# Kernel optimization log

Measured on AMD Instinct MI355X. Metric: run time of the kernel, lower is better.

Reference implementation:

```python
import jax, jax.numpy as jnp
import numpy as np

GAMMA = 0.99
EPS = 1e-8
N = 16777216  # flattened reward count


def setup_inputs() -> dict:
    key = jax.random.key(0)
    rewards = jax.random.normal(key, (N,), dtype=jnp.float32)
    return {"rewards": rewards}


def reference(rewards):
    # Sequential recurrence: R_t = gamma*R_{t-1} + r_t, Welford stats over R_t,
    # scaled[i] = r_i / max(std_t, eps), std_t = sqrt(var_sum/count) (1.0 if count < 2).
    flat = rewards.reshape(-1)

    def step(carry, r):
        R, cnt, mean, var_sum = carry
        R = GAMMA * R + r
        cnt = cnt + 1.0
        delta = R - mean
        mean = mean + delta / cnt
        var_sum = var_sum + delta * (R - mean)
        std = jnp.where(cnt < 2.0, jnp.float32(1.0), jnp.sqrt(var_sum / cnt))
        std = jnp.maximum(std, jnp.float32(EPS))
        return (R, cnt, mean, var_sum), r / std

    init = (jnp.float32(0.0), jnp.float32(0.0), jnp.float32(0.0), jnp.float32(0.0))
    _, scaled = jax.lax.scan(step, init, flat)
    return scaled.reshape(rewards.shape)
```

## Files before the change

### kernel.cpp

```cpp
#include <hip/hip_runtime.h>
#include <math.h>

#define THREADS 256
#define GAMMA 0.99

typedef float vf4 __attribute__((ext_vector_type(4)));

template<int LPT>
__device__ __forceinline__ int padi(int i) { return i + (i >> LPT); }

template<int NW>
__device__ __forceinline__ void block_compose_excl(int tid, double g, double v,
                                                   double& eg, double& ev,
                                                   double* lg, double* lv) {
    const int lane = tid & 63, wave = tid >> 6;
    double ig = g, iv = v;
#pragma unroll
    for (int k = 1; k < 64; k <<= 1) {
        double og = __shfl_up(ig, k);
        double ov = __shfl_up(iv, k);
        if (lane >= k) { iv = fma(ig, ov, iv); ig *= og; }
    }
    double weg = __shfl_up(ig, 1);
    double wev = __shfl_up(iv, 1);
    if (lane == 0) { weg = 1.0; wev = 0.0; }
    if (lane == 63) { lg[wave] = ig; lv[wave] = iv; }
    __syncthreads();
    double bg = 1.0, bv = 0.0;
    for (int w = 0; w < wave; ++w) { bv = fma(lg[w], bv, lv[w]); bg *= lg[w]; }
    eg = weg * bg;
    ev = fma(weg, bv, wev);
}

template<int NW>
__device__ __forceinline__ void block_add_excl2(int tid, double a, double b,
                                                double& ea, double& eb,
                                                double* la, double* lb) {
    const int lane = tid & 63, wave = tid >> 6;
    double ia = a, ib = b;
#pragma unroll
    for (int k = 1; k < 64; k <<= 1) {
        double oa = __shfl_up(ia, k);
        double ob = __shfl_up(ib, k);
        if (lane >= k) { ia += oa; ib += ob; }
    }
    double wea = __shfl_up(ia, 1);
    double web = __shfl_up(ib, 1);
    if (lane == 0) { wea = 0.0; web = 0.0; }
    if (lane == 63) { la[wave] = ia; lb[wave] = ib; }
    __syncthreads();
    double ba = 0.0, bb = 0.0;
    for (int w = 0; w < wave; ++w) { ba += la[w]; bb += lb[w]; }
    ea = wea + ba;
    eb = web + bb;
}

template<int PT, int LPT>
__global__ __launch_bounds__(THREADS) void rs_phase1(const float* __restrict__ in,
                                                     double* __restrict__ agg, int nchunk) {
    constexpr int CHUNKE = THREADS * PT;
    __shared__ double lg[4], lv[4], r1[4], r2[4], r3[4];
    const int tid = threadIdx.x, lane = tid & 63, wave = tid >> 6;
    const int chunk = blockIdx.x;
    const float* src = in + (size_t)chunk * CHUNKE + (size_t)tid * PT;

    float rv[PT];
#pragma unroll
    for (int q = 0; q < PT / 4; ++q) {
        const float4 t = ((const float4*)src)[q];
        rv[4 * q] = t.x; rv[4 * q + 1] = t.y; rv[4 * q + 2] = t.z; rv[4 * q + 3] = t.w;
    }
    const float gf = (float)GAMMA;
    float p = 0.f, psum = 0.f, pq = 0.f, p2 = 0.f, gp = 1.f;
#pragma unroll
    for (int j = 0; j < PT; ++j) {
        p = fmaf(gf, p, rv[j]);
        gp *= gf;
        psum += p;
        pq = fmaf(gp, p, pq);
        p2 = fmaf(p, p, p2);
    }
    const double g = GAMMA;
    double gPT = g;
#pragma unroll
    for (int e = 0; e < LPT; ++e) gPT *= gPT;

    double eg, ev;
    block_compose_excl<4>(tid, gPT, (double)p, eg, ev, lg, lv);
    const double rho = ev, gexc = eg;

    const double G1 = g * (1.0 - gPT) / (1.0 - g);
    const double G2 = g * g * (1.0 - gPT * gPT) / (1.0 - g * g);
    double c1 = fma(rho, G1, (double)psum);
    double c2 = gexc * fma(rho, G2, (double)pq);
    double c3 = fma(rho * rho, G2, fma(2.0 * rho, (double)pq, (double)p2));
#pragma unroll
    for (int k = 32; k > 0; k >>= 1) {
        c1 += __shfl_down(c1, k);
        c2 += __shfl_down(c2, k);
        c3 += __shfl_down(c3, k);
    }
    if (lane == 0) { r1[wave] = c1; r2[wave] = c2; r3[wave] = c3; }
    __syncthreads();
    if (tid == 0) {
        double A = 0.0;
#pragma unroll
        for (int w = 0; w < 4; ++w) A = fma(lg[w], A, lv[w]);
        agg[4 * (size_t)chunk + 0] = A;
        agg[4 * (size_t)chunk + 1] = r1[0] + r1[1] + r1[2] + r1[3];
        agg[4 * (size_t)chunk + 2] = r2[0] + r2[1] + r2[2] + r2[3];
        agg[4 * (size_t)chunk + 3] = r3[0] + r3[1] + r3[2] + r3[3];
    }
}

template<int CPT, int LOG2CHUNK>
__global__ __launch_bounds__(1024) void rs_phase2(const double* __restrict__ agg,
                                                  double* __restrict__ car, int nchunk) {
    __shared__ double lg[16], lv[16], la[16], lb[16];
    const int t = threadIdx.x;
    const double g = GAMMA;
    double gC = g;
#pragma unroll
    for (int e = 0; e < LOG2CHUNK; ++e) gC *= gC;

    double A[CPT], Ps[CPT], Pq[CPT], P2[CPT];
    const int c0 = t * CPT;
#pragma unroll
    for (int i = 0; i < CPT; ++i) {
        const int c = c0 + i;
        const bool ok = c < nchunk;
        A[i]  = ok ? agg[4 * (size_t)c + 0] : 0.0;
        Ps[i] = ok ? agg[4 * (size_t)c + 1] : 0.0;
        Pq[i] = ok ? agg[4 * (size_t)c + 2] : 0.0;
        P2[i] = ok ? agg[4 * (size_t)c + 3] : 0.0;
    }
    double mg = 1.0, mv = 0.0;
#pragma unroll
    for (int i = 0; i < CPT; ++i) { mv = fma(gC, mv, A[i]); mg *= gC; }

    double eg, ev;
    block_compose_excl<16>(t, mg, mv, eg, ev, lg, lv);

    const double G1C = g * (1.0 - gC) / (1.0 - g);
    const double G2C = g * g * (1.0 - gC * gC) / (1.0 - g * g);
    double Rin[CPT + 1];
    Rin[0] = ev;
    double s1[CPT], s2[CPT];
#pragma unroll
    for (int i = 0; i < CPT; ++i) {
        s1[i] = fma(Rin[i], G1C, Ps[i]);
        s2[i] = fma(Rin[i] * Rin[i], G2C, fma(2.0 * Rin[i], Pq[i], P2[i]));
        Rin[i + 1] = fma(gC, Rin[i], A[i]);
    }
    double ts1 = 0.0, ts2 = 0.0;
#pragma unroll
    for (int i = 0; i < CPT; ++i) { ts1 += s1[i]; ts2 += s2[i]; }
    double ea, eb;
    block_add_excl2<16>(t, ts1, ts2, ea, eb, la, lb);
#pragma unroll
    for (int i = 0; i < CPT; ++i) {
        const int c = c0 + i;
        if (c < nchunk) {
            car[3 * (size_t)c + 0] = Rin[i];
            car[3 * (size_t)c + 1] = ea;
            car[3 * (size_t)c + 2] = eb;
        }
        ea += s1[i];
        eb += s2[i];
    }
}

template<int PT, int LPT>
__global__ __launch_bounds__(THREADS) void rs_phase3(const float* __restrict__ in,
                                                     float* __restrict__ out,
                                                     const double* __restrict__ car, int nchunk) {
    constexpr int CHUNKE = THREADS * PT;
    __shared__ float sbuf[CHUNKE + THREADS];
    __shared__ double lg[4], lv[4], la[4], lb[4];
    const int tid = threadIdx.x;
    const int chunk = blockIdx.x;
    const float* src = in + (size_t)chunk * CHUNKE + (size_t)tid * PT;

    float rv[PT];
#pragma unroll
    for (int q = 0; q < PT / 4; ++q) {
        const float4 t = ((const float4*)src)[q];
        rv[4 * q] = t.x; rv[4 * q + 1] = t.y; rv[4 * q + 2] = t.z; rv[4 * q + 3] = t.w;
    }
    const float gf = (float)GAMMA;
    float p = 0.f, psum = 0.f, pq = 0.f, p2 = 0.f, gp = 1.f;
#pragma unroll
    for (int j = 0; j < PT; ++j) {
        p = fmaf(gf, p, rv[j]);
        gp *= gf;
        psum += p;
        pq = fmaf(gp, p, pq);
        p2 = fmaf(p, p, p2);
    }
    const double g = GAMMA;
    double gPT = g;
#pragma unroll
    for (int e = 0; e < LPT; ++e) gPT *= gPT;

    double eg, ev;
    block_compose_excl<4>(tid, gPT, (double)p, eg, ev, lg, lv);

    const double RinC = car[3 * (size_t)chunk + 0];
    const double S1C  = car[3 * (size_t)chunk + 1];
    const double S2C  = car[3 * (size_t)chunk + 2];
    const double rin  = fma(eg, RinC, ev);

    const double G1 = g * (1.0 - gPT) / (1.0 - g);
    const double G2 = g * g * (1.0 - gPT * gPT) / (1.0 - g * g);
    const double s1 = fma(rin, G1, (double)psum);
    const double s2 = fma(rin * rin, G2, fma(2.0 * rin, (double)pq, (double)p2));
    double ea, eb;
    block_add_excl2<4>(tid, s1, s2, ea, eb, la, lb);
    const double S1b = S1C + ea;
    const double S2b = S2C + eb;

    const int a0 = padi<LPT>(tid * PT);

    if (chunk == 0) {
        double R = rin, S1 = S1b, S2 = S2b;
        const size_t gbase = (size_t)tid * PT;
        for (int j = 0; j < PT; ++j) {
            const float rf = rv[j];
            R = fma(g, R, (double)rf);
            S1 += R;
            S2 = fma(R, R, S2);
            float ov;
            if (gbase + j == 0) {
                ov = rf;
            } else {
                const double cnt = (double)(gbase + j + 1);
                const double inv = 1.0 / cnt;
                const double mean = S1 * inv;
                double var = fma(S2, inv, -(mean * mean));
                var = var > 0.0 ? var : 0.0;
                double sd = sqrt(var);
                sd = sd > 1e-8 ? sd : 1e-8;
                ov = (float)((double)rf / sd);
            }
            sbuf[a0 + j] = ov;
        }
    } else {
        float R = (float)rin;
        float ls1 = 0.f, ls2 = 0.f;
        const float S1bf = (float)S1b, S2bf = (float)S2b;
        const float base_cnt = (float)((size_t)chunk * CHUNKE + (size_t)tid * PT);
#pragma unroll
        for (int j = 0; j < PT; ++j) {
            const float rf = rv[j];
            R = fmaf(gf, R, rf);
            ls1 += R;
            ls2 = fmaf(R, R, ls2);
            const float cnt = base_cnt + (float)(j + 1);
            const float S1f = S1bf + ls1;
            const float S2f = S2bf + ls2;
            float t = fmaf(S2f, cnt, -(S1f * S1f));
            t = fmaxf(t, 1e-12f);
            sbuf[a0 + j] = rf * cnt * __builtin_amdgcn_rsqf(t);
        }
    }
    __syncthreads();

    float* dst = out + (size_t)chunk * CHUNKE;
    for (int i = tid * 4; i < CHUNKE; i += THREADS * 4) {
        const int pp = padi<LPT>(i);
        vf4 v;
        v.x = sbuf[pp]; v.y = sbuf[pp + 1]; v.z = sbuf[pp + 2]; v.w = sbuf[pp + 3];
        __builtin_nontemporal_store(v, (vf4*)(dst + i));
    }
}

extern "C" void kernel_launch(void* const* d_in, const int* in_sizes, int n_in,
                              void* d_out, int out_size, void* d_ws, size_t ws_size,
                              hipStream_t stream) {
    (void)n_in; (void)out_size;
    const float* in = (const float*)d_in[0];
    float* out = (float*)d_out;
    double* ws = (double*)d_ws;
    const int n = in_sizes[0];

    const int nc = n / 4096;
    if ((n % 4096) == 0 && nc >= 1 && nc <= 4096 &&
        ws_size >= (size_t)7 * nc * sizeof(double)) {
        double* agg = ws;
        double* car = ws + 4 * (size_t)nc;
        rs_phase1<16, 4><<<nc, THREADS, 0, stream>>>(in, agg, nc);
        rs_phase2<4, 12><<<1, 1024, 0, stream>>>(agg, car, nc);
        rs_phase3<16, 4><<<nc, THREADS, 0, stream>>>(in, out, car, nc);
    } else {
        const int nc64 = n / 16384;
        double* agg = ws;
        double* car = ws + 4 * (size_t)nc64;
        rs_phase1<64, 6><<<nc64, THREADS, 0, stream>>>(in, agg, nc64);
        rs_phase2<4, 14><<<1, 1024, 0, stream>>>(agg, car, nc64);
        rs_phase3<64, 6><<<nc64, THREADS, 0, stream>>>(in, out, car, nc64);
    }
}
```

Measured before the change: 55.02 us.

## Fuse chunk-carry scan into phase-1 kernel via last-block atomic counter

Merges the separate single-block carry-scan kernel into the tail of the per-chunk aggregation kernel. Each block increments a global counter after writing its aggregates, and the last block to finish performs the cross-chunk scan and writes the carries. This removes one kernel launch and its dependency gap. In exchange it adds a memset launch and does the scan with 256 threads instead of 1024, so each thread has a longer serial loop and reads the aggregates from global memory twice.

```diff
diff --git a/kernel.cpp b/kernel.cpp
--- a/kernel.cpp
+++ b/kernel.cpp
@@ -55,11 +55,14 @@
     eb = web + bb;
 }
 
-template<int PT, int LPT>
-__global__ __launch_bounds__(THREADS) void rs_phase1(const float* __restrict__ in,
-                                                     double* __restrict__ agg, int nchunk) {
+template<int PT, int LPT, int LOG2CH>
+__global__ __launch_bounds__(THREADS) void rs_phase12(const float* __restrict__ in,
+                                                      double* __restrict__ agg,
+                                                      double* __restrict__ car,
+                                                      int* __restrict__ counter, int nchunk) {
     constexpr int CHUNKE = THREADS * PT;
-    __shared__ double lg[4], lv[4], r1[4], r2[4], r3[4];
+    __shared__ double lg[4], lv[4], r1[4], r2[4], r3[4], la[4], lb[4];
+    __shared__ int is_last;
     const int tid = threadIdx.x, lane = tid & 63, wave = tid >> 6;
     const int chunk = blockIdx.x;
     const float* src = in + (size_t)chunk * CHUNKE + (size_t)tid * PT;
@@ -110,63 +113,54 @@
         agg[4 * (size_t)chunk + 1] = r1[0] + r1[1] + r1[2] + r1[3];
         agg[4 * (size_t)chunk + 2] = r2[0] + r2[1] + r2[2] + r2[3];
         agg[4 * (size_t)chunk + 3] = r3[0] + r3[1] + r3[2] + r3[3];
-    }
-}
-
-template<int CPT, int LOG2CHUNK>
-__global__ __launch_bounds__(1024) void rs_phase2(const double* __restrict__ agg,
-                                                  double* __restrict__ car, int nchunk) {
-    __shared__ double lg[16], lv[16], la[16], lb[16];
-    const int t = threadIdx.x;
-    const double g = GAMMA;
+        __threadfence();
+        const int prev = atomicAdd(counter, 1);
+        is_last = (prev == nchunk - 1) ? 1 : 0;
+    }
+    __syncthreads();
+    if (!is_last) return;
+
+    __threadfence();
     double gC = g;
 #pragma unroll
-    for (int e = 0; e < LOG2CHUNK; ++e) gC *= gC;
-
-    double A[CPT], Ps[CPT], Pq[CPT], P2[CPT];
-    const int c0 = t * CPT;
-#pragma unroll
-    for (int i = 0; i < CPT; ++i) {
-        const int c = c0 + i;
-        const bool ok = c < nchunk;
-        A[i]  = ok ? agg[4 * (size_t)c + 0] : 0.0;
-        Ps[i] = ok ? agg[4 * (size_t)c + 1] : 0.0;
-        Pq[i] = ok ? agg[4 * (size_t)c + 2] : 0.0;
-        P2[i] = ok ? agg[4 * (size_t)c + 3] : 0.0;
-    }
-    double mg = 1.0, mv = 0.0;
-#pragma unroll
-    for (int i = 0; i < CPT; ++i) { mv = fma(gC, mv, A[i]); mg *= gC; }
-
-    double eg, ev;
-    block_compose_excl<16>(t, mg, mv, eg, ev, lg, lv);
-
+    for (int e = 0; e < LOG2CH; ++e) gC *= gC;
     const double G1C = g * (1.0 - gC) / (1.0 - g);
     const double G2C = g * g * (1.0 - gC * gC) / (1.0 - g * g);
-    double Rin[CPT + 1];
-    Rin[0] = ev;
-    double s1[CPT], s2[CPT];
-#pragma unroll
-    for (int i = 0; i < CPT; ++i) {
-        s1[i] = fma(Rin[i], G1C, Ps[i]);
-        s2[i] = fma(Rin[i] * Rin[i], G2C, fma(2.0 * Rin[i], Pq[i], P2[i]));
-        Rin[i + 1] = fma(gC, Rin[i], A[i]);
-    }
-    double ts1 = 0.0, ts2 = 0.0;
-#pragma unroll
-    for (int i = 0; i < CPT; ++i) { ts1 += s1[i]; ts2 += s2[i]; }
+
+    const int CPT2 = (nchunk + THREADS - 1) / THREADS;
+    const int b_lo = tid * CPT2;
+    const int b_hi = min(nchunk, b_lo + CPT2);
+
+    double mg = 1.0, mv = 0.0;
+    for (int c = b_lo; c < b_hi; ++c) { mv = fma(gC, mv, agg[4 * (size_t)c]); mg *= gC; }
+    double eg2, ev2;
+    block_compose_excl<4>(tid, mg, mv, eg2, ev2, lg, lv);
+
+    double Rin = ev2, ts1 = 0.0, ts2 = 0.0;
+    for (int c = b_lo; c < b_hi; ++c) {
+        const double Ac = agg[4 * (size_t)c + 0];
+        const double Ps = agg[4 * (size_t)c + 1];
+        const double Pq = agg[4 * (size_t)c + 2];
+        const double P2 = agg[4 * (size_t)c + 3];
+        ts1 += fma(Rin, G1C, Ps);
+        ts2 += fma(Rin * Rin, G2C, fma(2.0 * Rin, Pq, P2));
+        Rin = fma(gC, Rin, Ac);
+    }
     double ea, eb;
-    block_add_excl2<16>(t, ts1, ts2, ea, eb, la, lb);
-#pragma unroll
-    for (int i = 0; i < CPT; ++i) {
-        const int c = c0 + i;
-        if (c < nchunk) {
-            car[3 * (size_t)c + 0] = Rin[i];
-            car[3 * (size_t)c + 1] = ea;
-            car[3 * (size_t)c + 2] = eb;
-        }
-        ea += s1[i];
-        eb += s2[i];
+    block_add_excl2<4>(tid, ts1, ts2, ea, eb, la, lb);
+
+    Rin = ev2;
+    for (int c = b_lo; c < b_hi; ++c) {
+        const double Ac = agg[4 * (size_t)c + 0];
+        const double Ps = agg[4 * (size_t)c + 1];
+        const double Pq = agg[4 * (size_t)c + 2];
+        const double P2 = agg[4 * (size_t)c + 3];
+        car[3 * (size_t)c + 0] = Rin;
+        car[3 * (size_t)c + 1] = ea;
+        car[3 * (size_t)c + 2] = eb;
+        ea += fma(Rin, G1C, Ps);
+        eb += fma(Rin * Rin, G2C, fma(2.0 * Rin, Pq, P2));
+        Rin = fma(gC, Rin, Ac);
     }
 }
 
@@ -285,18 +279,20 @@
 
     const int nc = n / 4096;
     if ((n % 4096) == 0 && nc >= 1 && nc <= 4096 &&
-        ws_size >= (size_t)7 * nc * sizeof(double)) {
+        ws_size >= (size_t)7 * nc * sizeof(double) + sizeof(int)) {
         double* agg = ws;
         double* car = ws + 4 * (size_t)nc;
-        rs_phase1<16, 4><<<nc, THREADS, 0, stream>>>(in, agg, nc);
-        rs_phase2<4, 12><<<1, 1024, 0, stream>>>(agg, car, nc);
+        int* counter = (int*)(ws + 7 * (size_t)nc);
+        hipMemsetAsync(counter, 0, sizeof(int), stream);
+        rs_phase12<16, 4, 12><<<nc, THREADS, 0, stream>>>(in, agg, car, counter, nc);
         rs_phase3<16, 4><<<nc, THREADS, 0, stream>>>(in, out, car, nc);
     } else {
         const int nc64 = n / 16384;
         double* agg = ws;
         double* car = ws + 4 * (size_t)nc64;
-        rs_phase1<64, 6><<<nc64, THREADS, 0, stream>>>(in, agg, nc64);
-        rs_phase2<4, 14><<<1, 1024, 0, stream>>>(agg, car, nc64);
+        int* counter = (int*)(ws + 7 * (size_t)nc64);
+        hipMemsetAsync(counter, 0, sizeof(int), stream);
+        rs_phase12<64, 6, 14><<<nc64, THREADS, 0, stream>>>(in, agg, car, counter, nc64);
         rs_phase3<64, 6><<<nc64, THREADS, 0, stream>>>(in, out, car, nc64);
     }
 }
```

New measurement: 148.2 us. 169% more time.
